# Performance work log

Measured on AMD Instinct MI355X. Metric: run time of the kernel, lower is better.

The kernel has to match this reference:

```python
import jax, jax.numpy as jnp
import numpy as np
import itertools

B, H, W, C = 64, 28, 28, 576
NH, WS = 18, 7
KD = C // NH          # head dim = 32 (attn_ratio=1 so d == key_dim)
HID = 4 * C           # mlp hidden
N = WS * WS           # tokens per window = 49


def _bias_idxs():
    points = list(itertools.product(range(WS), range(WS)))
    offsets, idxs = {}, []
    for p1 in points:
        for p2 in points:
            off = (abs(p1[0] - p2[0]), abs(p1[1] - p2[1]))
            if off not in offsets:
                offsets[off] = len(offsets)
            idxs.append(offsets[off])
    return np.asarray(idxs, dtype=np.int64).reshape(N, N), len(offsets)


def setup_inputs() -> dict:
    key = jax.random.key(0)
    ks = jax.random.split(key, 10)
    idxs, n_off = _bias_idxs()  # n_off == 49
    s = 0.02
    return {
        "x": jax.random.normal(ks[0], (B, H * W, C), jnp.float32),
        "gamma_a": jnp.ones((C,), jnp.float32),
        "beta_a": jnp.zeros((C,), jnp.float32),
        "qkv_w": jax.random.normal(ks[1], (3 * C, C), jnp.float32) * s,
        "qkv_b": jnp.zeros((3 * C,), jnp.float32),
        "proj_w": jax.random.normal(ks[2], (C, C), jnp.float32) * s,
        "proj_b": jnp.zeros((C,), jnp.float32),
        "attn_biases": jax.random.normal(ks[3], (NH, n_off), jnp.float32) * s,
        "conv_w": jax.random.normal(ks[4], (C, 1, 3, 3), jnp.float32) * 0.1,
        "bn_gamma": jnp.ones((C,), jnp.float32),
        "bn_beta": jnp.zeros((C,), jnp.float32),
        "bn_mean": jnp.zeros((C,), jnp.float32),
        "bn_var": jax.random.uniform(ks[5], (C,), jnp.float32, 0.5, 1.5),
        "gamma_m": jnp.ones((C,), jnp.float32),
        "beta_m": jnp.zeros((C,), jnp.float32),
        "fc1_w": jax.random.normal(ks[6], (HID, C), jnp.float32) * s,
        "fc1_b": jnp.zeros((HID,), jnp.float32),
        "fc2_w": jax.random.normal(ks[7], (C, HID), jnp.float32) * s,
        "fc2_b": jnp.zeros((C,), jnp.float32),
        "bias_idxs": jnp.asarray(idxs),
    }


def _ln(x, g, b, eps=1e-5):
    mu = x.mean(-1, keepdims=True)
    var = ((x - mu) ** 2).mean(-1, keepdims=True)
    return (x - mu) * jax.lax.rsqrt(var + eps) * g + b


def reference(x, gamma_a, beta_a, qkv_w, qkv_b, proj_w, proj_b, attn_biases,
              conv_w, bn_gamma, bn_beta, bn_mean, bn_var,
              gamma_m, beta_m, fc1_w, fc1_b, fc2_w, fc2_b, bias_idxs):
    scale = KD ** -0.5
    nWh, nWw = H // WS, W // WS
    res = x
    # ---- window partition: (B, H*W, C) -> (B*nWh*nWw, 49, C) ----
    xw = x.reshape(B, nWh, WS, nWw, WS, C).transpose(0, 1, 3, 2, 4, 5)
    xw = xw.reshape(-1, N, C)
    # ---- windowed attention with gathered relative-position bias ----
    h = _ln(xw, gamma_a, beta_a)
    qkv = h @ qkv_w.T + qkv_b                       # (Bw, N, 3C)
    qkv = qkv.reshape(-1, N, NH, 3 * KD)
    q, k, v = jnp.split(qkv, 3, axis=-1)            # each (Bw, N, NH, KD)
    q = q.transpose(0, 2, 1, 3)
    k = k.transpose(0, 2, 1, 3)
    v = v.transpose(0, 2, 1, 3)
    bias = attn_biases[:, bias_idxs]                # (NH, N, N)
    attn = jnp.einsum('bhnd,bhmd->bhnm', q, k) * scale + bias
    attn = jax.nn.softmax(attn, axis=-1)
    out = jnp.einsum('bhnm,bhmd->bhnd', attn, v)    # (Bw, NH, N, KD)
    out = out.transpose(0, 2, 1, 3).reshape(-1, N, C) @ proj_w.T + proj_b
    # ---- window reverse ----
    out = out.reshape(B, nWh, nWw, WS, WS, C).transpose(0, 1, 3, 2, 4, 5)
    out = out.reshape(B, H * W, C)
    x = res + out
    # ---- depthwise 3x3 conv + BatchNorm (inference stats) ----
    xc = x.transpose(0, 2, 1).reshape(B, C, H, W)
    xc = jax.lax.conv_general_dilated(
        xc, conv_w, (1, 1), [(1, 1), (1, 1)],
        feature_group_count=C,
        dimension_numbers=('NCHW', 'OIHW', 'NCHW'))
    eps = 1e-5
    inv = (jax.lax.rsqrt(bn_var + eps) * bn_gamma)[:, None, None]
    xc = (xc - bn_mean[:, None, None]) * inv + bn_beta[:, None, None]
    x = xc.reshape(B, C, H * W).transpose(0, 2, 1)
    # ---- MLP with pre-LayerNorm ----
    hm = _ln(x, gamma_m, beta_m)
    hm = jax.nn.gelu(hm @ fc1_w.T + fc1_b, approximate=False)
    hm = hm @ fc2_w.T + fc2_b
    return x + hm
```

## Files before the change

### kernel.cpp

```cpp
#include <hip/hip_runtime.h>
#include <hip/hip_bf16.h>

typedef __bf16 v8bf  __attribute__((ext_vector_type(8)));
typedef __bf16 v4bf  __attribute__((ext_vector_type(4)));
typedef float  f32x4 __attribute__((ext_vector_type(4)));
typedef float  f32x8 __attribute__((ext_vector_type(8)));

#define TOKENS 50176
#define CDIM   576
#define NHEAD  18
#define QKVD   1728

__device__ __forceinline__ void gld16(const __bf16* g, __bf16* l)
{
    __builtin_amdgcn_global_load_lds(
        (const __attribute__((address_space(1))) void*)g,
        (__attribute__((address_space(3))) void*)l,
        16, 0, 0);
}

__device__ __forceinline__ float fast_gelu(float x)
{
    const float z  = x * 0.70710678118654752f;
    const float az = fabsf(z);
    const float t  = __frcp_rn(1.0f + 0.3275911f * az);
    float p = 1.061405429f;
    p = p * t - 1.453152027f;
    p = p * t + 1.421413741f;
    p = p * t - 0.284496736f;
    p = p * t + 0.254829592f;
    const float e   = __expf(-z * z);
    float erfv = 1.0f - p * t * e;
    erfv = copysignf(erfv, z);
    return 0.5f * x * (1.0f + erfv);
}

__global__ __launch_bounds__(256)
void cast_kernel(const float* __restrict__ in, __bf16* __restrict__ out)
{
    const size_t i = ((size_t)blockIdx.x * 256 + threadIdx.x) * 4;
    f32x4 v = *(const f32x4*)&in[i];
    v4bf o;
#pragma unroll
    for (int j = 0; j < 4; ++j) o[j] = (__bf16)v[j];
    *(v4bf*)&out[i] = o;
}

__global__ __launch_bounds__(64)
void conv_prep(const float* __restrict__ w, const float* __restrict__ bg,
               const float* __restrict__ bb, const float* __restrict__ bm,
               const float* __restrict__ bv, __bf16* __restrict__ wt,
               float* __restrict__ bias2)
{
    const int c = blockIdx.x * 64 + threadIdx.x;
    const float inv = rsqrtf(bv[c] + 1e-5f) * bg[c];
#pragma unroll
    for (int t = 0; t < 9; ++t) wt[t * CDIM + c] = (__bf16)(w[c * 9 + t] * inv);
    bias2[c] = bb[c] - bm[c] * inv;
}

template<typename InT>
__global__ __launch_bounds__(256)
void ln_kernel(const InT* __restrict__ x, const float* __restrict__ g,
               const float* __restrict__ b, __bf16* __restrict__ out)
{
    const int lane = threadIdx.x & 63;
    const int wid  = threadIdx.x >> 6;
    const size_t t = (size_t)blockIdx.x * 4 + wid;
    const InT* row = x + t * CDIM;

    float v[16];
    float sum = 0.f, sq = 0.f;
    if constexpr (sizeof(InT) == 2) {
        v8bf d0 = *(const v8bf*)&row[(size_t)lane * 8];
#pragma unroll
        for (int j = 0; j < 8; ++j) { float f = (float)d0[j]; v[j] = f; sum += f; sq += f * f; }
    } else {
        f32x8 d0 = *(const f32x8*)&row[(size_t)lane * 8];
#pragma unroll
        for (int j = 0; j < 8; ++j) { float f = d0[j]; v[j] = f; sum += f; sq += f * f; }
    }
    if (lane < 8) {
        if constexpr (sizeof(InT) == 2) {
            v8bf d1 = *(const v8bf*)&row[(size_t)(lane + 64) * 8];
#pragma unroll
            for (int j = 0; j < 8; ++j) { float f = (float)d1[j]; v[8 + j] = f; sum += f; sq += f * f; }
        } else {
            f32x8 d1 = *(const f32x8*)&row[(size_t)(lane + 64) * 8];
#pragma unroll
            for (int j = 0; j < 8; ++j) { float f = d1[j]; v[8 + j] = f; sum += f; sq += f * f; }
        }
    }
#pragma unroll
    for (int o = 32; o >= 1; o >>= 1) {
        sum += __shfl_xor(sum, o, 64);
        sq  += __shfl_xor(sq,  o, 64);
    }
    const float mean = sum * (1.0f / CDIM);
    const float rstd = rsqrtf(sq * (1.0f / CDIM) - mean * mean + 1e-5f);

    {
        int c0 = lane * 8;
        v8bf o0;
#pragma unroll
        for (int j = 0; j < 8; ++j)
            o0[j] = (__bf16)((v[j] - mean) * rstd * g[c0 + j] + b[c0 + j]);
        *(v8bf*)&out[t * CDIM + c0] = o0;
    }
    if (lane < 8) {
        int c0 = (lane + 64) * 8;
        v8bf o1;
#pragma unroll
        for (int j = 0; j < 8; ++j)
            o1[j] = (__bf16)((v[8 + j] - mean) * rstd * g[c0 + j] + b[c0 + j]);
        *(v8bf*)&out[t * CDIM + c0] = o1;
    }
}

template<int EPI, typename OutT, typename AddT>
__global__ __launch_bounds__(512, 1)
void gemm_bt(const __bf16* __restrict__ A, const __bf16* __restrict__ W,
             const float* __restrict__ bias, const AddT* __restrict__ add,
             OutT* __restrict__ C, int N, int K, int nN)
{
    constexpr int BK = 32;
    constexpr int ASZ = 256 * BK;
    constexpr int BSZ = 192 * BK;
    __shared__ __bf16 L[3][ASZ + BSZ];
    const int tid = threadIdx.x, lane = tid & 63, wid = tid >> 6;
    const int lr = lane & 15, kh = lane >> 4;
    const int wm = wid >> 2, wn = wid & 3;

    const int nwg = gridDim.x, bid = blockIdx.x;
    const int q = nwg >> 3, r = nwg & 7;
    const int xcd = bid & 7, jc = bid >> 3;
    const int wgid = (xcd < r ? xcd * (q + 1) : r * (q + 1) + (xcd - r) * q) + jc;
    const int mblk = wgid / nN, nblk = wgid - mblk * nN;
    const int m0 = mblk * 256, n0 = nblk * 192;

    const __bf16* pA = A + (size_t)(m0 + wid * 32 + lr) * K + kh * 8;
    const __bf16* pW = W + (size_t)(n0 + (wid < 6 ? wid : 0) * 32 + lr) * K + kh * 8;

    auto stageA = [&](int s, int kt) {
#pragma unroll
        for (int i = 0; i < 2; ++i)
            gld16(pA + (size_t)(i * 16) * K + kt * BK, &L[s][(wid * 2 + i) * 512]);
    };
    auto stageB = [&](int s, int kt) {
        if (wid < 6) {
#pragma unroll
            for (int i = 0; i < 2; ++i)
                gld16(pW + (size_t)(i * 16) * K + kt * BK,
                      &L[s][ASZ + (wid * 2 + i) * 512]);
        }
    };

    const int lo = lane * 8;

    f32x4 acc[8][3] = {};
    const int NT = K / BK;

    stageA(0, 0); stageB(0, 0);
    stageA(1, 1); stageB(1, 1);

    for (int t = 0; t < NT; ++t) {
        if (t + 1 < NT) {
            if (wid < 6) asm volatile("s_waitcnt vmcnt(4)" ::: "memory");
            else         asm volatile("s_waitcnt vmcnt(2)" ::: "memory");
        } else {
            asm volatile("s_waitcnt vmcnt(0)" ::: "memory");
        }
        __builtin_amdgcn_s_barrier();

        const __bf16* Ls = L[t % 3];

        v8bf b_[3], a_[4];
#pragma unroll
        for (int nf = 0; nf < 3; ++nf)
            b_[nf] = *(const v8bf*)&Ls[ASZ + (wn * 3 + nf) * 512 + lo];
#pragma unroll
        for (int mf = 0; mf < 4; ++mf)
            a_[mf] = *(const v8bf*)&Ls[(wm * 8 + mf) * 512 + lo];

        if (t + 2 < NT) stageA((t + 2) % 3, t + 2);

        __builtin_amdgcn_s_barrier();

        __builtin_amdgcn_s_setprio(1);
#pragma unroll
        for (int mf = 0; mf < 4; ++mf)
#pragma unroll
            for (int nf = 0; nf < 3; ++nf)
                acc[mf][nf] = __builtin_amdgcn_mfma_f32_16x16x32_bf16(
                    a_[mf], b_[nf], acc[mf][nf], 0, 0, 0);
        __builtin_amdgcn_s_setprio(0);

        v8bf a2_[4];
#pragma unroll
        for (int mf = 0; mf < 4; ++mf)
            a2_[mf] = *(const v8bf*)&Ls[(wm * 8 + 4 + mf) * 512 + lo];

        if (t + 2 < NT) stageB((t + 2) % 3, t + 2);

        __builtin_amdgcn_s_barrier();

        __builtin_amdgcn_s_setprio(1);
#pragma unroll
        for (int mf = 0; mf < 4; ++mf)
#pragma unroll
            for (int nf = 0; nf < 3; ++nf)
                acc[4 + mf][nf] = __builtin_amdgcn_mfma_f32_16x16x32_bf16(
                    a2_[mf], b_[nf], acc[4 + mf][nf], 0, 0, 0);
        __builtin_amdgcn_s_setprio(0);
    }

#pragma unroll
    for (int mf = 0; mf < 8; ++mf)
#pragma unroll
        for (int nf = 0; nf < 3; ++nf)
#pragma unroll
            for (int rr = 0; rr < 4; ++rr) {
                int row = m0 + wm * 128 + mf * 16 + kh * 4 + rr;
                int col = n0 + wn * 48 + nf * 16 + lr;
                float vv = acc[mf][nf][rr] + bias[col];
                if (EPI == 1) vv += (float)add[(size_t)row * N + col];
                if (EPI == 2) vv = fast_gelu(vv);
                C[(size_t)row * N + col] = (OutT)vv;
            }
}

__global__ __launch_bounds__(64)
void attn_kernel(const __bf16* __restrict__ qkv, const float* __restrict__ biases,
                 const int* __restrict__ bidx, __bf16* __restrict__ out)
{
    const int head = blockIdx.x;
    const int win  = blockIdx.y;
    const int tid  = threadIdx.x;
    const int b  = win >> 4;
    const int wy = (win >> 2) & 3;
    const int wx = win & 3;
    __shared__ float kk[49][32];
    __shared__ float vv[49][32];
    const size_t hb = (size_t)head * 96;

    for (int e = tid; e < 49 * 32; e += 64) {
        int n = e >> 5, d = e & 31;
        int iy = n / 7, ix = n - iy * 7;
        size_t t = (size_t)b * 784 + (size_t)(wy * 7 + iy) * 28 + wx * 7 + ix;
        const __bf16* p = qkv + t * QKVD + hb;
        kk[n][d] = (float)p[32 + d];
        vv[n][d] = (float)p[64 + d];
    }
    float q[32];
    size_t tmine = 0;
    if (tid < 49) {
        int iy = tid / 7, ix = tid - iy * 7;
        tmine = (size_t)b * 784 + (size_t)(wy * 7 + iy) * 28 + wx * 7 + ix;
        const __bf16* p = qkv + tmine * QKVD + hb;
#pragma unroll
        for (int d = 0; d < 32; ++d) q[d] = (float)p[d];
    }
    __syncthreads();
    if (tid >= 49) return;

    const float scale = 0.17677669529663687f;
    float s[49];
    float mx = -1e30f;
    const int*   brow = bidx + tid * 49;
    const float* bh   = biases + head * 49;
#pragma unroll
    for (int m = 0; m < 49; ++m) {
        float dot = 0.f;
#pragma unroll
        for (int d = 0; d < 32; ++d) dot += q[d] * kk[m][d];
        float val = dot * scale + bh[brow[m]];
        s[m] = val;
        mx = fmaxf(mx, val);
    }
    float sum = 0.f;
#pragma unroll
    for (int m = 0; m < 49; ++m) { float e = __expf(s[m] - mx); s[m] = e; sum += e; }
    const float rs = 1.0f / sum;

    __bf16* op = out + tmine * CDIM + (size_t)head * 32;
#pragma unroll
    for (int d = 0; d < 32; ++d) {
        float a = 0.f;
#pragma unroll
        for (int m = 0; m < 49; ++m) a += s[m] * vv[m][d];
        op[d] = (__bf16)(a * rs);
    }
}

__global__ __launch_bounds__(256)
void conv_bn_v(const __bf16* __restrict__ xin, const __bf16* __restrict__ wt,
               const float* __restrict__ bias2, __bf16* __restrict__ xout)
{
    const size_t gt = (size_t)blockIdx.x * 256 + threadIdx.x;
    const int g = (int)(gt % 72);
    const size_t p = gt / 72;
    const int bimg = (int)(p / 784);
    const int pix  = (int)(p - (size_t)bimg * 784);
    const int y = pix / 28, xx = pix - y * 28;
    const int c0 = g * 8;

    float acc[8];
    {
        f32x4 b0 = *(const f32x4*)&bias2[c0];
        f32x4 b1 = *(const f32x4*)&bias2[c0 + 4];
#pragma unroll
        for (int jj = 0; jj < 4; ++jj) { acc[jj] = b0[jj]; acc[4 + jj] = b1[jj]; }
    }
#pragma unroll
    for (int dy = 0; dy < 3; ++dy) {
        int ny = y + dy - 1;
        if (ny < 0 || ny >= 28) continue;
#pragma unroll
        for (int dx = 0; dx < 3; ++dx) {
            int nx = xx + dx - 1;
            if (nx < 0 || nx >= 28) continue;
            v8bf xv = *(const v8bf*)&xin[((size_t)bimg * 784 + ny * 28 + nx) * CDIM + c0];
            v8bf wv = *(const v8bf*)&wt[(dy * 3 + dx) * CDIM + c0];
#pragma unroll
            for (int jj = 0; jj < 8; ++jj) acc[jj] += (float)xv[jj] * (float)wv[jj];
        }
    }
    v8bf o;
#pragma unroll
    for (int jj = 0; jj < 8; ++jj) o[jj] = (__bf16)acc[jj];
    *(v8bf*)&xout[p * CDIM + c0] = o;
}

extern "C" void kernel_launch(void* const* d_in, const int* in_sizes, int n_in,
                              void* d_out, int out_size, void* d_ws, size_t ws_size,
                              hipStream_t stream)
{
    (void)in_sizes; (void)n_in; (void)out_size; (void)ws_size;
    const float* x          = (const float*)d_in[0];
    const float* gamma_a    = (const float*)d_in[1];
    const float* beta_a     = (const float*)d_in[2];
    const float* qkv_w      = (const float*)d_in[3];
    const float* qkv_b      = (const float*)d_in[4];
    const float* proj_w     = (const float*)d_in[5];
    const float* proj_b     = (const float*)d_in[6];
    const float* attn_bias  = (const float*)d_in[7];
    const float* conv_w     = (const float*)d_in[8];
    const float* bn_g       = (const float*)d_in[9];
    const float* bn_b       = (const float*)d_in[10];
    const float* bn_m       = (const float*)d_in[11];
    const float* bn_v       = (const float*)d_in[12];
    const float* gamma_m    = (const float*)d_in[13];
    const float* beta_m     = (const float*)d_in[14];
    const float* fc1_w      = (const float*)d_in[15];
    const float* fc1_b      = (const float*)d_in[16];
    const float* fc2_w      = (const float*)d_in[17];
    const float* fc2_b      = (const float*)d_in[18];
    const int*   bidx       = (const int*)d_in[19];

    const size_t T = TOKENS;
    __bf16* ws     = (__bf16*)d_ws;
    __bf16* hbuf   = ws;
    __bf16* qkvbuf = ws + T * 576;
    __bf16* aout   = ws;
    __bf16* x2     = ws + T * 2304;
    __bf16* x3     = x2 + T * 576;
    __bf16* lnm    = x2;
    __bf16* f1     = ws;
    __bf16* wq     = x3 + T * 576;
    __bf16* wp     = wq + (size_t)QKVD * CDIM;
    __bf16* w1     = wp + (size_t)CDIM * CDIM;
    __bf16* w2     = w1 + (size_t)2304 * CDIM;
    __bf16* wt     = w2 + (size_t)CDIM * 2304;
    float*  bias2  = (float*)(wt + 9 * CDIM);
    float*  outp   = (float*)d_out;

    cast_kernel<<<dim3((QKVD * CDIM) / 1024), 256, 0, stream>>>(qkv_w, wq);
    cast_kernel<<<dim3((CDIM * CDIM) / 1024), 256, 0, stream>>>(proj_w, wp);
    cast_kernel<<<dim3((2304 * CDIM) / 1024), 256, 0, stream>>>(fc1_w, w1);
    cast_kernel<<<dim3((CDIM * 2304) / 1024), 256, 0, stream>>>(fc2_w, w2);
    conv_prep<<<dim3(9), 64, 0, stream>>>(conv_w, bn_g, bn_b, bn_m, bn_v, wt, bias2);

    ln_kernel<float><<<dim3(T / 4), 256, 0, stream>>>(x, gamma_a, beta_a, hbuf);
    gemm_bt<0, __bf16, float><<<dim3(196 * 9), 512, 0, stream>>>(
        hbuf, wq, qkv_b, nullptr, qkvbuf, QKVD, CDIM, 9);
    attn_kernel<<<dim3(NHEAD, 1024), 64, 0, stream>>>(qkvbuf, attn_bias, bidx, aout);
    gemm_bt<1, __bf16, float><<<dim3(196 * 3), 512, 0, stream>>>(
        aout, wp, proj_b, x, x2, CDIM, CDIM, 3);
    conv_bn_v<<<dim3(14112), 256, 0, stream>>>(x2, wt, bias2, x3);
    ln_kernel<__bf16><<<dim3(T / 4), 256, 0, stream>>>(x3, gamma_m, beta_m, lnm);
    gemm_bt<2, __bf16, float><<<dim3(196 * 12), 512, 0, stream>>>(
        lnm, w1, fc1_b, nullptr, f1, 2304, CDIM, 12);
    gemm_bt<1, float, __bf16><<<dim3(196 * 3), 512, 0, stream>>>(
        f1, w2, fc2_b, x3, outp, CDIM, 2304, 3);
}
```

Before: 1.025 ms.

## Restructure GEMM to BK=64 double buffering with 4x2 wave tiling

The bf16 GEMM moves from a triple-buffered BK=32 pipeline with a 2x4 wave grid (each wave 128x48) to a double-buffered BK=64 pipeline with a 4x2 wave grid (each wave 64x96). Each k-step loads A and B fragments into registers and reuses them across four MFMA phases, which halves the number of outer iterations. It also balances global-to-LDS staging across all 8 waves in 7 rounds. The trade-off is a full vmcnt(0) wait plus more barriers per iteration, so prefetch depth drops to one stage and load latency may be less well hidden.

```diff
diff --git a/kernel.cpp b/kernel.cpp
--- a/kernel.cpp
+++ b/kernel.cpp
@@ -123,13 +123,13 @@
              const float* __restrict__ bias, const AddT* __restrict__ add,
              OutT* __restrict__ C, int N, int K, int nN)
 {
-    constexpr int BK = 32;
+    constexpr int BK  = 64;
     constexpr int ASZ = 256 * BK;
-    constexpr int BSZ = 192 * BK;
-    __shared__ __bf16 L[3][ASZ + BSZ];
+    constexpr int BUF = ASZ + 192 * BK;
+    __shared__ __bf16 L[2][BUF];
     const int tid = threadIdx.x, lane = tid & 63, wid = tid >> 6;
     const int lr = lane & 15, kh = lane >> 4;
-    const int wm = wid >> 2, wn = wid & 3;
+    const int wm = wid >> 1, wn = wid & 1;
 
     const int nwg = gridDim.x, bid = blockIdx.x;
     const int q = nwg >> 3, r = nwg & 7;
@@ -138,90 +138,116 @@
     const int mblk = wgid / nN, nblk = wgid - mblk * nN;
     const int m0 = mblk * 256, n0 = nblk * 192;
 
-    const __bf16* pA = A + (size_t)(m0 + wid * 32 + lr) * K + kh * 8;
-    const __bf16* pW = W + (size_t)(n0 + (wid < 6 ? wid : 0) * 32 + lr) * K + kh * 8;
-
-    auto stageA = [&](int s, int kt) {
-#pragma unroll
-        for (int i = 0; i < 2; ++i)
-            gld16(pA + (size_t)(i * 16) * K + kt * BK, &L[s][(wid * 2 + i) * 512]);
-    };
-    auto stageB = [&](int s, int kt) {
-        if (wid < 6) {
-#pragma unroll
-            for (int i = 0; i < 2; ++i)
-                gld16(pW + (size_t)(i * 16) * K + kt * BK,
-                      &L[s][ASZ + (wid * 2 + i) * 512]);
+    auto stageRound = [&](int s, int kt, int j) {
+        if (j < 4) {
+            const int c = wid + 8 * j;
+            gld16(A + (size_t)(m0 + (c >> 1) * 16 + lr) * K
+                    + kt * BK + (c & 1) * 32 + kh * 8,
+                  &L[s][c * 512]);
+        } else {
+            const int c = wid + 8 * (j - 4);
+            gld16(W + (size_t)(n0 + (c >> 1) * 16 + lr) * K
+                    + kt * BK + (c & 1) * 32 + kh * 8,
+                  &L[s][ASZ + c * 512]);
         }
     };
 
     const int lo = lane * 8;
 
-    f32x4 acc[8][3] = {};
+    f32x4 acc[4][6] = {};
     const int NT = K / BK;
 
-    stageA(0, 0); stageB(0, 0);
-    stageA(1, 1); stageB(1, 1);
+#pragma unroll
+    for (int j = 0; j < 7; ++j) stageRound(0, 0, j);
 
     for (int t = 0; t < NT; ++t) {
-        if (t + 1 < NT) {
-            if (wid < 6) asm volatile("s_waitcnt vmcnt(4)" ::: "memory");
-            else         asm volatile("s_waitcnt vmcnt(2)" ::: "memory");
-        } else {
-            asm volatile("s_waitcnt vmcnt(0)" ::: "memory");
+        const int cur = t & 1;
+        asm volatile("s_waitcnt vmcnt(0)" ::: "memory");
+        __builtin_amdgcn_s_barrier();
+
+        const __bf16* Ls = L[cur];
+        const bool pf = (t + 1 < NT);
+        v8bf b0[6], b1[6], a[2];
+
+#pragma unroll
+        for (int nf = 0; nf < 6; ++nf)
+            b0[nf] = *(const v8bf*)&Ls[ASZ + ((wn * 6 + nf) * 2 + 0) * 512 + lo];
+#pragma unroll
+        for (int mf = 0; mf < 2; ++mf)
+            a[mf] = *(const v8bf*)&Ls[((wm * 4 + mf) * 2 + 0) * 512 + lo];
+        if (pf) {
+            stageRound(cur ^ 1, t + 1, 0); stageRound(cur ^ 1, t + 1, 1);
+            stageRound(cur ^ 1, t + 1, 2); stageRound(cur ^ 1, t + 1, 3);
         }
         __builtin_amdgcn_s_barrier();
-
-        const __bf16* Ls = L[t % 3];
-
-        v8bf b_[3], a_[4];
-#pragma unroll
-        for (int nf = 0; nf < 3; ++nf)
-            b_[nf] = *(const v8bf*)&Ls[ASZ + (wn * 3 + nf) * 512 + lo];
-#pragma unroll
-        for (int mf = 0; mf < 4; ++mf)
-            a_[mf] = *(const v8bf*)&Ls[(wm * 8 + mf) * 512 + lo];
-
-        if (t + 2 < NT) stageA((t + 2) % 3, t + 2);
-
-        __builtin_amdgcn_s_barrier();
-
         __builtin_amdgcn_s_setprio(1);
 #pragma unroll
-        for (int mf = 0; mf < 4; ++mf)
-#pragma unroll
-            for (int nf = 0; nf < 3; ++nf)
+        for (int mf = 0; mf < 2; ++mf)
+#pragma unroll
+            for (int nf = 0; nf < 6; ++nf)
                 acc[mf][nf] = __builtin_amdgcn_mfma_f32_16x16x32_bf16(
-                    a_[mf], b_[nf], acc[mf][nf], 0, 0, 0);
+                    a[mf], b0[nf], acc[mf][nf], 0, 0, 0);
         __builtin_amdgcn_s_setprio(0);
-
-        v8bf a2_[4];
-#pragma unroll
-        for (int mf = 0; mf < 4; ++mf)
-            a2_[mf] = *(const v8bf*)&Ls[(wm * 8 + 4 + mf) * 512 + lo];
-
-        if (t + 2 < NT) stageB((t + 2) % 3, t + 2);
-
-        __builtin_amdgcn_s_barrier();
-
+        __builtin_amdgcn_s_barrier();
+
+#pragma unroll
+        for (int nf = 0; nf < 6; ++nf)
+            b1[nf] = *(const v8bf*)&Ls[ASZ + ((wn * 6 + nf) * 2 + 1) * 512 + lo];
+#pragma unroll
+        for (int mf = 0; mf < 2; ++mf)
+            a[mf] = *(const v8bf*)&Ls[((wm * 4 + mf) * 2 + 1) * 512 + lo];
+        if (pf) {
+            stageRound(cur ^ 1, t + 1, 4); stageRound(cur ^ 1, t + 1, 5);
+            stageRound(cur ^ 1, t + 1, 6);
+        }
+        __builtin_amdgcn_s_barrier();
         __builtin_amdgcn_s_setprio(1);
 #pragma unroll
-        for (int mf = 0; mf < 4; ++mf)
-#pragma unroll
-            for (int nf = 0; nf < 3; ++nf)
-                acc[4 + mf][nf] = __builtin_amdgcn_mfma_f32_16x16x32_bf16(
-                    a2_[mf], b_[nf], acc[4 + mf][nf], 0, 0, 0);
+        for (int mf = 0; mf < 2; ++mf)
+#pragma unroll
+            for (int nf = 0; nf < 6; ++nf)
+                acc[mf][nf] = __builtin_amdgcn_mfma_f32_16x16x32_bf16(
+                    a[mf], b1[nf], acc[mf][nf], 0, 0, 0);
         __builtin_amdgcn_s_setprio(0);
-    }
-
-#pragma unroll
-    for (int mf = 0; mf < 8; ++mf)
-#pragma unroll
-        for (int nf = 0; nf < 3; ++nf)
+        __builtin_amdgcn_s_barrier();
+
+#pragma unroll
+        for (int mf = 0; mf < 2; ++mf)
+            a[mf] = *(const v8bf*)&Ls[((wm * 4 + 2 + mf) * 2 + 0) * 512 + lo];
+        __builtin_amdgcn_s_barrier();
+        __builtin_amdgcn_s_setprio(1);
+#pragma unroll
+        for (int mf = 0; mf < 2; ++mf)
+#pragma unroll
+            for (int nf = 0; nf < 6; ++nf)
+                acc[2 + mf][nf] = __builtin_amdgcn_mfma_f32_16x16x32_bf16(
+                    a[mf], b0[nf], acc[2 + mf][nf], 0, 0, 0);
+        __builtin_amdgcn_s_setprio(0);
+        __builtin_amdgcn_s_barrier();
+
+#pragma unroll
+        for (int mf = 0; mf < 2; ++mf)
+            a[mf] = *(const v8bf*)&Ls[((wm * 4 + 2 + mf) * 2 + 1) * 512 + lo];
+        __builtin_amdgcn_s_barrier();
+        __builtin_amdgcn_s_setprio(1);
+#pragma unroll
+        for (int mf = 0; mf < 2; ++mf)
+#pragma unroll
+            for (int nf = 0; nf < 6; ++nf)
+                acc[2 + mf][nf] = __builtin_amdgcn_mfma_f32_16x16x32_bf16(
+                    a[mf], b1[nf], acc[2 + mf][nf], 0, 0, 0);
+        __builtin_amdgcn_s_setprio(0);
+        __builtin_amdgcn_s_barrier();
+    }
+
+#pragma unroll
+    for (int mf = 0; mf < 4; ++mf)
+#pragma unroll
+        for (int nf = 0; nf < 6; ++nf)
 #pragma unroll
             for (int rr = 0; rr < 4; ++rr) {
-                int row = m0 + wm * 128 + mf * 16 + kh * 4 + rr;
-                int col = n0 + wn * 48 + nf * 16 + lr;
+                int row = m0 + wm * 64 + mf * 16 + kh * 4 + rr;
+                int col = n0 + wn * 96 + nf * 16 + lr;
                 float vv = acc[mf][nf][rr] + bias[col];
                 if (EPI == 1) vv += (float)add[(size_t)row * N + col];
                 if (EPI == 2) vv = fast_gelu(vv);
```

Measured after the change: 1.119 ms. 1.09x slower.
